# Optimization experiments

Hardware: AMD Instinct MI355X
Metric: run time of the kernel (lower is better)

## Reference

```python
import jax, jax.numpy as jnp
import numpy as np

N_NODES = 100000
N_EDGES = 1600000
IN_DIM = 48
HID = 128
BN_EPS = 1e-5


def _batchnorm(h, gamma, beta):
    # BatchNorm1d in training mode: batch mean, biased variance
    mu = jnp.mean(h, axis=0)
    var = jnp.mean(jnp.square(h - mu), axis=0)
    return (h - mu) * jax.lax.rsqrt(var + BN_EPS) * gamma + beta


def setup_inputs() -> dict:
    key = jax.random.key(0)
    ks = jax.random.split(key, 8)
    x = jax.random.normal(ks[0], (N_NODES, IN_DIM), dtype=jnp.float32)
    edge_index = jax.random.randint(ks[1], (2, N_EDGES), 0, N_NODES, dtype=jnp.int64)
    s1 = 1.0 / np.sqrt(IN_DIM)
    s2 = 1.0 / np.sqrt(HID)
    return {
        "x": x,
        "edge_index": edge_index,
        "W1": jax.random.uniform(ks[2], (HID, IN_DIM), jnp.float32, -s1, s1),
        "b1": jnp.zeros((HID,), jnp.float32),
        "g1": jnp.ones((HID,), jnp.float32),
        "be1": jnp.zeros((HID,), jnp.float32),
        "Wl": jax.random.uniform(ks[3], (HID, HID), jnp.float32, -s2, s2),
        "bl": jnp.zeros((HID,), jnp.float32),
        "Wr": jax.random.uniform(ks[4], (HID, HID), jnp.float32, -s2, s2),
        "g2": jnp.ones((HID,), jnp.float32),
        "be2": jnp.zeros((HID,), jnp.float32),
    }


def reference(x, edge_index, W1, b1, g1, be1, Wl, bl, Wr, g2, be2):
    # input projection: Linear -> BatchNorm -> ReLU
    h = x @ W1.T + b1                               # [N, HID]
    feat = jax.nn.relu(_batchnorm(h, g1, be1))      # [N, HID]

    # SAGEConv (mean aggregation): messages flow src -> dst
    src, dst = edge_index[0], edge_index[1]
    summed = jax.ops.segment_sum(feat[src], dst, num_segments=N_NODES)  # [N, HID]
    cnt = jax.ops.segment_sum(jnp.ones((N_EDGES,), jnp.float32), dst, num_segments=N_NODES)
    agg = summed / jnp.maximum(cnt, 1.0)[:, None]
    sage = agg @ Wl.T + bl + feat @ Wr.T            # lin_l(mean) + lin_r(self)

    out_feat = _batchnorm(sage, g2, be2)
    return (feat, out_feat)
```

## Files before the change

kernel.cpp:

```cpp
#include <hip/hip_runtime.h>
#include <hip/hip_bf16.h>

#define NN 100000
#define NE 1600000
#define INDIM 48
#define HID 128
#define K2 256
#define KP 64
#define BN_EPS 1e-5f

#define NBUK 782
#define BCAP 2816
#define CHUNK 8192
#define NBB 196
#define NPRJ 320

#define MT2 ((NN + 127) / 128)

typedef short s8v __attribute__((ext_vector_type(8)));
typedef float f4v __attribute__((ext_vector_type(4)));
typedef float f2v __attribute__((ext_vector_type(2)));

__device__ __forceinline__ unsigned short f2bf(float f) {
    __hip_bfloat16 b = __float2bfloat16(f);
    unsigned short u;
    __builtin_memcpy(&u, &b, 2);
    return u;
}
__device__ __forceinline__ float bflo(unsigned u) { return __uint_as_float(u << 16); }
__device__ __forceinline__ float bfhi(unsigned u) { return __uint_as_float(u & 0xffff0000u); }
__device__ __forceinline__ unsigned packbf(float lo, float hi) {
    return (unsigned)f2bf(lo) | ((unsigned)f2bf(hi) << 16);
}

__global__ __launch_bounds__(512) void k_prep_proj(const int* __restrict__ ei,
                                                   int* __restrict__ bcur,
                                                   unsigned int* __restrict__ bbuf,
                                                   const float* __restrict__ x,
                                                   const float* __restrict__ W1,
                                                   const float* __restrict__ b1,
                                                   unsigned short* __restrict__ Abuf,
                                                   float* __restrict__ colSum,
                                                   float* __restrict__ colSq) {
  union __align__(16) SMem {
    struct {
      int cnt[1024];
      int sc[2][1024];
      int ofs[1024];
      int lcur[1024];
      int gbase[1024];
      unsigned int stag[CHUNK];
      unsigned short sbkt[CHUNK];
    } p;
    struct {
      unsigned short Bsh[HID][KP + 8];
      float redS[8][HID];
      float redQ[8][HID];
    } g;
  };
  __shared__ SMem sm;
  int tid = threadIdx.x;

  if (blockIdx.x < NBB) {
    int base = blockIdx.x * CHUNK;
    int lim = min(CHUNK, NE - base);
    sm.p.cnt[tid] = 0;
    sm.p.cnt[tid + 512] = 0;
    __syncthreads();
#pragma unroll
    for (int i = 0; i < CHUNK / 512; ++i) {
      int e = i * 512 + tid;
      if (e < lim) {
        int d = ei[NE + base + e];
        d = min(max(d, 0), NN - 1);
        atomicAdd(&sm.p.cnt[d >> 7], 1);
      }
    }
    __syncthreads();
    sm.p.sc[0][tid] = sm.p.cnt[tid];
    sm.p.sc[0][tid + 512] = sm.p.cnt[tid + 512];
    __syncthreads();
    int pp = 0;
    for (int d = 1; d < 1024; d <<= 1) {
      int a0 = sm.p.sc[pp][tid];
      int a1 = sm.p.sc[pp][tid + 512];
      if (tid >= d) a0 += sm.p.sc[pp][tid - d];
      a1 += sm.p.sc[pp][tid + 512 - d];
      sm.p.sc[pp ^ 1][tid] = a0;
      sm.p.sc[pp ^ 1][tid + 512] = a1;
      __syncthreads();
      pp ^= 1;
    }
    sm.p.ofs[tid] = sm.p.sc[pp][tid] - sm.p.cnt[tid];
    sm.p.ofs[tid + 512] = sm.p.sc[pp][tid + 512] - sm.p.cnt[tid + 512];
    sm.p.lcur[tid] = sm.p.ofs[tid];
    sm.p.lcur[tid + 512] = sm.p.ofs[tid + 512];
    if (tid < NBUK) sm.p.gbase[tid] = atomicAdd(&bcur[tid], sm.p.cnt[tid]);
    if (tid + 512 < NBUK) sm.p.gbase[tid + 512] = atomicAdd(&bcur[tid + 512], sm.p.cnt[tid + 512]);
    __syncthreads();
#pragma unroll
    for (int i = 0; i < CHUNK / 512; ++i) {
      int e = i * 512 + tid;
      if (e < lim) {
        int s = ei[base + e];
        int d = ei[NE + base + e];
        s = min(max(s, 0), NN - 1);
        d = min(max(d, 0), NN - 1);
        int b = d >> 7;
        int pos = atomicAdd(&sm.p.lcur[b], 1);
        sm.p.stag[pos] = (unsigned)s | ((unsigned)(d & 127) << 17);
        sm.p.sbkt[pos] = (unsigned short)b;
      }
    }
    __syncthreads();
    for (int s = tid; s < lim; s += 512) {
      int b = sm.p.sbkt[s];
      int off = sm.p.gbase[b] + (s - sm.p.ofs[b]);
      if (off < BCAP) bbuf[(size_t)b * BCAP + off] = sm.p.stag[s];
    }
    return;
  }

  int bid2 = blockIdx.x - NBB;
  for (int i = tid; i < HID * KP; i += 512) {
    int j = i >> 6, k = i & (KP - 1);
    sm.g.Bsh[j][k] = (k < INDIM) ? f2bf(W1[j * INDIM + k]) : (unsigned short)0;
  }
  __syncthreads();
  int w = tid >> 6, l = tid & 63;
  int m16 = l & 15, q = l >> 4;
  float bcol[8];
#pragma unroll
  for (int nt = 0; nt < 8; ++nt) bcol[nt] = b1[nt * 16 + m16];
  float ssum[8], ssq[8];
#pragma unroll
  for (int nt = 0; nt < 8; ++nt) { ssum[nt] = 0.f; ssq[nt] = 0.f; }
  f4v zero4 = {0.f, 0.f, 0.f, 0.f};
  s8v zero8 = {0, 0, 0, 0, 0, 0, 0, 0};
  for (int tile = bid2; tile < MT2; tile += NPRJ) {
    int row = tile * 128 + w * 16 + m16;
    bool rv = row < NN;
    const float* xr = x + (size_t)row * INDIM;
    f4v acc[8];
#pragma unroll
    for (int nt = 0; nt < 8; ++nt) acc[nt] = zero4;
#pragma unroll
    for (int kt = 0; kt < 2; ++kt) {
      int c0 = kt * 32 + q * 8;
      s8v a = zero8;
      if (rv && c0 < INDIM) {
        float4 v0 = *(const float4*)(xr + c0);
        float4 v1 = *(const float4*)(xr + c0 + 4);
        a[0] = (short)f2bf(v0.x); a[1] = (short)f2bf(v0.y);
        a[2] = (short)f2bf(v0.z); a[3] = (short)f2bf(v0.w);
        a[4] = (short)f2bf(v1.x); a[5] = (short)f2bf(v1.y);
        a[6] = (short)f2bf(v1.z); a[7] = (short)f2bf(v1.w);
      }
#pragma unroll
      for (int nt = 0; nt < 8; ++nt) {
        s8v b = *(const s8v*)(&sm.g.Bsh[nt * 16 + m16][kt * 32 + q * 8]);
        acc[nt] = __builtin_amdgcn_mfma_f32_16x16x32_bf16(a, b, acc[nt], 0, 0, 0);
      }
    }
    int rbase = tile * 128 + w * 16 + q * 4;
#pragma unroll
    for (int nt = 0; nt < 8; ++nt) {
      int col = nt * 16 + m16;
#pragma unroll
      for (int r4 = 0; r4 < 4; ++r4) {
        int rr = rbase + r4;
        if (rr < NN) {
          float v = acc[nt][r4] + bcol[nt];
          Abuf[(size_t)rr * K2 + HID + col] = f2bf(v);
          ssum[nt] += v;
          ssq[nt] = fmaf(v, v, ssq[nt]);
        }
      }
    }
  }
#pragma unroll
  for (int nt = 0; nt < 8; ++nt) {
    float s = ssum[nt], qq = ssq[nt];
    s += __shfl_xor(s, 16);
    s += __shfl_xor(s, 32);
    qq += __shfl_xor(qq, 16);
    qq += __shfl_xor(qq, 32);
    if (q == 0) {
      sm.g.redS[w][nt * 16 + m16] = s;
      sm.g.redQ[w][nt * 16 + m16] = qq;
    }
  }
  __syncthreads();
  if (tid < HID) {
    float s = 0.f, qq = 0.f;
#pragma unroll
    for (int ww = 0; ww < 8; ++ww) { s += sm.g.redS[ww][tid]; qq += sm.g.redQ[ww][tid]; }
    atomicAdd(&colSum[tid], s);
    atomicAdd(&colSq[tid], qq);
  }
}

__global__ __launch_bounds__(256) void k_apply(float* __restrict__ feat,
                                               const float* __restrict__ colSum,
                                               const float* __restrict__ colSq,
                                               const float* __restrict__ g1,
                                               const float* __restrict__ be1,
                                               unsigned short* __restrict__ A,
                                               unsigned char* __restrict__ feat8) {
  __shared__ __align__(16) float sa[HID], sb[HID];
  int tid = threadIdx.x;
  if (tid < HID) {
    float mu = colSum[tid] * (1.0f / NN);
    float var = fmaxf(colSq[tid] * (1.0f / NN) - mu * mu, 0.f);
    float a = g1[tid] * rsqrtf(var + BN_EPS);
    sa[tid] = a;
    sb[tid] = be1[tid] - mu * a;
  }
  __syncthreads();
  int i = blockIdx.x * 256 + tid;
  if (i >= NN * 16) return;
  int r = i >> 4, c8 = (i & 15) << 3;
  unsigned short* ap = A + (size_t)r * K2 + HID + c8;
  uint4 hv = *(const uint4*)ap;
  float4 a0 = *(const float4*)(sa + c8);
  float4 a1 = *(const float4*)(sa + c8 + 4);
  float4 b0 = *(const float4*)(sb + c8);
  float4 b1 = *(const float4*)(sb + c8 + 4);
  float f0 = fmaxf(fmaf(bflo(hv.x), a0.x, b0.x), 0.f);
  float f1 = fmaxf(fmaf(bfhi(hv.x), a0.y, b0.y), 0.f);
  float f2 = fmaxf(fmaf(bflo(hv.y), a0.z, b0.z), 0.f);
  float f3 = fmaxf(fmaf(bfhi(hv.y), a0.w, b0.w), 0.f);
  float f4 = fmaxf(fmaf(bflo(hv.z), a1.x, b1.x), 0.f);
  float f5 = fmaxf(fmaf(bfhi(hv.z), a1.y, b1.y), 0.f);
  float f6 = fmaxf(fmaf(bflo(hv.w), a1.z, b1.z), 0.f);
  float f7 = fmaxf(fmaf(bfhi(hv.w), a1.w, b1.w), 0.f);
  float4 o0 = {f0, f1, f2, f3}, o1 = {f4, f5, f6, f7};
  *(float4*)(feat + (size_t)r * HID + c8) = o0;
  *(float4*)(feat + (size_t)r * HID + c8 + 4) = o1;
  uint4 ob;
  ob.x = packbf(f0, f1);
  ob.y = packbf(f2, f3);
  ob.z = packbf(f4, f5);
  ob.w = packbf(f6, f7);
  *(uint4*)ap = ob;
  unsigned p0 = __builtin_amdgcn_cvt_pk_fp8_f32(f0, f1, 0u, false);
  p0 = __builtin_amdgcn_cvt_pk_fp8_f32(f2, f3, p0, true);
  unsigned p1 = __builtin_amdgcn_cvt_pk_fp8_f32(f4, f5, 0u, false);
  p1 = __builtin_amdgcn_cvt_pk_fp8_f32(f6, f7, p1, true);
  uint2 o8 = {p0, p1};
  *(uint2*)(feat8 + (size_t)r * HID + c8) = o8;
}

__global__ __launch_bounds__(512) void k_bucket_agg(const unsigned int* __restrict__ bbuf,
                                                    const int* __restrict__ bcnt,
                                                    const unsigned char* __restrict__ feat8,
                                                    unsigned short* __restrict__ Abuf) {
  __shared__ unsigned int lcsr[BCAP];
  __shared__ int cnt[128], ofs[128], cur[128];
  __shared__ int sc[2][128];
  int tid = threadIdx.x;
  int b = blockIdx.x;
  int m = min(bcnt[b], BCAP);
  int n0 = b << 7;
  int nb = min(128, NN - n0);
  if (tid < 128) cnt[tid] = 0;
  __syncthreads();
  const unsigned int* bp = bbuf + (size_t)b * BCAP;
  for (int s = tid; s < m; s += 512) {
    unsigned p = bp[s];
    atomicAdd(&cnt[(p >> 17) & 127], 1);
  }
  __syncthreads();
  if (tid < 128) sc[0][tid] = cnt[tid];
  __syncthreads();
  int pp = 0;
  for (int d = 1; d < 128; d <<= 1) {
    if (tid < 128) {
      int v = sc[pp][tid];
      if (tid >= d) v += sc[pp][tid - d];
      sc[pp ^ 1][tid] = v;
    }
    __syncthreads();
    pp ^= 1;
  }
  if (tid < 128) {
    int o = sc[pp][tid] - cnt[tid];
    ofs[tid] = o;
    cur[tid] = o;
  }
  __syncthreads();
  for (int s = tid; s < m; s += 512) {
    unsigned p = bp[s];
    int ld = (p >> 17) & 127;
    int pos = atomicAdd(&cur[ld], 1);
    lcsr[pos] = p & 0x1FFFF;
  }
  __syncthreads();
  int lane = tid & 31;
  int g = tid >> 5;
  int half = (lane >> 3) & 3;
  int l8 = lane & 7;
  for (int ln = g; ln < nb; ln += 16) {
    int deg = cnt[ln], beg = ofs[ln];
    float ac[16];
#pragma unroll
    for (int i = 0; i < 16; ++i) ac[i] = 0.f;
#pragma unroll 2
    for (int j = 0; j < deg; j += 4) {
      int idx = j + half;
      uint4 v = {0u, 0u, 0u, 0u};
      if (idx < deg) {
        int s = lcsr[beg + idx];
        v = *(const uint4*)(feat8 + (size_t)s * HID + l8 * 16);
      }
      f2v d;
      d = __builtin_amdgcn_cvt_pk_f32_fp8(v.x, false); ac[0] += d.x;  ac[1] += d.y;
      d = __builtin_amdgcn_cvt_pk_f32_fp8(v.x, true);  ac[2] += d.x;  ac[3] += d.y;
      d = __builtin_amdgcn_cvt_pk_f32_fp8(v.y, false); ac[4] += d.x;  ac[5] += d.y;
      d = __builtin_amdgcn_cvt_pk_f32_fp8(v.y, true);  ac[6] += d.x;  ac[7] += d.y;
      d = __builtin_amdgcn_cvt_pk_f32_fp8(v.z, false); ac[8] += d.x;  ac[9] += d.y;
      d = __builtin_amdgcn_cvt_pk_f32_fp8(v.z, true);  ac[10] += d.x; ac[11] += d.y;
      d = __builtin_amdgcn_cvt_pk_f32_fp8(v.w, false); ac[12] += d.x; ac[13] += d.y;
      d = __builtin_amdgcn_cvt_pk_f32_fp8(v.w, true);  ac[14] += d.x; ac[15] += d.y;
    }
#pragma unroll
    for (int i = 0; i < 16; ++i) {
      ac[i] += __shfl_xor(ac[i], 8);
      ac[i] += __shfl_xor(ac[i], 16);
    }
    if (half == 0) {
      float inv = 1.f / fmaxf((float)deg, 1.f);
      uint4 o0, o1;
      o0.x = packbf(ac[0] * inv, ac[1] * inv);
      o0.y = packbf(ac[2] * inv, ac[3] * inv);
      o0.z = packbf(ac[4] * inv, ac[5] * inv);
      o0.w = packbf(ac[6] * inv, ac[7] * inv);
      o1.x = packbf(ac[8] * inv, ac[9] * inv);
      o1.y = packbf(ac[10] * inv, ac[11] * inv);
      o1.z = packbf(ac[12] * inv, ac[13] * inv);
      o1.w = packbf(ac[14] * inv, ac[15] * inv);
      unsigned short* op = Abuf + (size_t)(n0 + ln) * K2 + l8 * 16;
      *(uint4*)op = o0;
      *(uint4*)(op + 8) = o1;
    }
  }
}

__global__ __launch_bounds__(512) void k_gemm(
    const unsigned short* __restrict__ A,
    const float* __restrict__ Wl, const float* __restrict__ Wr,
    const float* __restrict__ bl, unsigned short* __restrict__ sageb,
    float* __restrict__ colSum, float* __restrict__ colSq) {
  __shared__ __align__(16) unsigned short Bsh[HID][264];
  __shared__ float redS[8][HID], redQ[8][HID];
  int tid = threadIdx.x;
  for (int i4 = tid; i4 < HID * K2 / 4; i4 += 512) {
    int i = i4 << 2;
    int j = i >> 8, k = i & (K2 - 1);
    const float* src = (k < HID) ? (Wl + j * HID + k) : (Wr + j * HID + (k - HID));
    float4 v = *(const float4*)src;
    uint2 u;
    u.x = packbf(v.x, v.y);
    u.y = packbf(v.z, v.w);
    *(uint2*)&Bsh[j][k] = u;
  }
  __syncthreads();
  int w = tid >> 6, l = tid & 63;
  int m16 = l & 15, q = l >> 4;
  int tile = blockIdx.x;
  int row = tile * 128 + w * 16 + m16;
  bool rv = row < NN;
  f4v zero4 = {0.f, 0.f, 0.f, 0.f};
  s8v zero8 = {0, 0, 0, 0, 0, 0, 0, 0};
  f4v acc[8];
#pragma unroll
  for (int nt = 0; nt < 8; ++nt) acc[nt] = zero4;
#pragma unroll
  for (int kt = 0; kt < 8; ++kt) {
    s8v a = zero8;
    if (rv) a = *(const s8v*)(A + (size_t)row * K2 + kt * 32 + q * 8);
#pragma unroll
    for (int nt = 0; nt < 8; ++nt) {
      s8v bfr = *(const s8v*)(&Bsh[nt * 16 + m16][kt * 32 + q * 8]);
      acc[nt] = __builtin_amdgcn_mfma_f32_16x16x32_bf16(a, bfr, acc[nt], 0, 0, 0);
    }
  }
  int rbase = tile * 128 + w * 16 + q * 4;
  float ssum[8], ssq[8];
#pragma unroll
  for (int nt = 0; nt < 8; ++nt) { ssum[nt] = 0.f; ssq[nt] = 0.f; }
#pragma unroll
  for (int nt = 0; nt < 8; ++nt) {
    int col = nt * 16 + m16;
    float bv = bl[col];
#pragma unroll
    for (int r4 = 0; r4 < 4; ++r4) {
      int rr = rbase + r4;
      if (rr < NN) {
        float v = acc[nt][r4] + bv;
        sageb[(size_t)rr * HID + col] = f2bf(v);
        ssum[nt] += v;
        ssq[nt] = fmaf(v, v, ssq[nt]);
      }
    }
  }
#pragma unroll
  for (int nt = 0; nt < 8; ++nt) {
    float s = ssum[nt], qq = ssq[nt];
    s += __shfl_xor(s, 16);
    s += __shfl_xor(s, 32);
    qq += __shfl_xor(qq, 16);
    qq += __shfl_xor(qq, 32);
    if (q == 0) {
      redS[w][nt * 16 + m16] = s;
      redQ[w][nt * 16 + m16] = qq;
    }
  }
  __syncthreads();
  if (tid < HID) {
    float s = 0.f, qq = 0.f;
#pragma unroll
    for (int ww = 0; ww < 8; ++ww) { s += redS[ww][tid]; qq += redQ[ww][tid]; }
    atomicAdd(&colSum[tid], s);
    atomicAdd(&colSq[tid], qq);
  }
}

__global__ __launch_bounds__(256) void k_bn_apply(const unsigned short* __restrict__ sageb,
                                                  float* __restrict__ out,
                                                  const float* __restrict__ colSum,
                                                  const float* __restrict__ colSq,
                                                  const float* __restrict__ g2,
                                                  const float* __restrict__ be2) {
  __shared__ __align__(16) float sa[HID], sb[HID];
  int tid = threadIdx.x;
  if (tid < HID) {
    float mu = colSum[tid] * (1.0f / NN);
    float var = fmaxf(colSq[tid] * (1.0f / NN) - mu * mu, 0.f);
    float a = g2[tid] * rsqrtf(var + BN_EPS);
    sa[tid] = a;
    sb[tid] = be2[tid] - mu * a;
  }
  __syncthreads();
  int i = blockIdx.x * 256 + tid;
  if (i >= NN * 16) return;
  int r = i >> 4, c8 = (i & 15) << 3;
  uint4 sv = *(const uint4*)(sageb + (size_t)r * HID + c8);
  float4 a0 = *(const float4*)(sa + c8);
  float4 a1 = *(const float4*)(sa + c8 + 4);
  float4 b0 = *(const float4*)(sb + c8);
  float4 b1 = *(const float4*)(sb + c8 + 4);
  float4 o0, o1;
  o0.x = fmaf(bflo(sv.x), a0.x, b0.x);
  o0.y = fmaf(bfhi(sv.x), a0.y, b0.y);
  o0.z = fmaf(bflo(sv.y), a0.z, b0.z);
  o0.w = fmaf(bfhi(sv.y), a0.w, b0.w);
  o1.x = fmaf(bflo(sv.z), a1.x, b1.x);
  o1.y = fmaf(bfhi(sv.z), a1.y, b1.y);
  o1.z = fmaf(bflo(sv.w), a1.z, b1.z);
  o1.w = fmaf(bfhi(sv.w), a1.w, b1.w);
  *(float4*)(out + (size_t)r * HID + c8) = o0;
  *(float4*)(out + (size_t)r * HID + c8 + 4) = o1;
}

extern "C" void kernel_launch(void* const* d_in, const int* in_sizes, int n_in,
                              void* d_out, int out_size, void* d_ws, size_t ws_size,
                              hipStream_t stream) {
  const float* x   = (const float*)d_in[0];
  const int*   ei  = (const int*)d_in[1];
  const float* W1  = (const float*)d_in[2];
  const float* b1  = (const float*)d_in[3];
  const float* g1  = (const float*)d_in[4];
  const float* be1 = (const float*)d_in[5];
  const float* Wl  = (const float*)d_in[6];
  const float* bl  = (const float*)d_in[7];
  const float* Wr  = (const float*)d_in[8];
  const float* g2  = (const float*)d_in[9];
  const float* be2 = (const float*)d_in[10];

  float* feat_out = (float*)d_out;
  float* out2     = (float*)d_out + (size_t)NN * HID;

  size_t off = 0;
  auto alloc = [&](size_t bytes) -> void* {
    void* p = (char*)d_ws + off;
    off += (bytes + 255) & ~(size_t)255;
    return p;
  };
  float*          stats = (float*)alloc(4 * HID * 4);
  int*            bcur  = (int*)alloc((size_t)NBUK * 4);
  unsigned short* Abuf  = (unsigned short*)alloc((size_t)NN * K2 * 2);
  unsigned char*  feat8 = (unsigned char*)alloc((size_t)NN * HID);
  unsigned short* sageb = (unsigned short*)alloc((size_t)NN * HID * 2);
  unsigned int*   bbuf  = (unsigned int*)alloc((size_t)NBUK * BCAP * 4);
  float* colSum1 = stats;
  float* colSq1  = stats + HID;
  float* colSum2 = stats + 2 * HID;
  float* colSq2  = stats + 3 * HID;

  hipMemsetAsync(stats, 0, 4 * HID * 4 + (size_t)NBUK * 4, stream);
  k_prep_proj<<<NBB + NPRJ, 512, 0, stream>>>(ei, bcur, bbuf, x, W1, b1, Abuf, colSum1, colSq1);
  k_apply<<<(NN * 16 + 255) / 256, 256, 0, stream>>>(feat_out, colSum1, colSq1, g1, be1, Abuf, feat8);
  k_bucket_agg<<<NBUK, 512, 0, stream>>>(bbuf, bcur, feat8, Abuf);
  k_gemm<<<MT2, 512, 0, stream>>>(Abuf, Wl, Wr, bl, sageb, colSum2, colSq2);
  k_bn_apply<<<(NN * 16 + 255) / 256, 256, 0, stream>>>(sageb, out2, colSum2, colSq2, g2, be2);
}
```

Baseline: 287.3 us.

## Fuse neighbor aggregation with SAGE GEMM, keep aggregated tile in LDS

Merges the bucket aggregation kernel and the SAGE GEMM into one kernel. Each block writes its 128-node mean-aggregated tile into shared memory and feeds it straight into MFMA, so the aggregate is never written to or read back from global memory. The self-feature buffer shrinks from 256 to 128 columns, and the concatenated Wl/Wr weights are converted to bf16 once by extra blocks in the prep kernel. In exchange, the GEMM now reads B fragments directly from global/L2 instead of LDS, and the fused kernel uses more shared memory and registers, which may reduce occupancy.

```diff
diff --git a/kernel.cpp b/kernel.cpp
--- a/kernel.cpp
+++ b/kernel.cpp
@@ -14,6 +14,7 @@
 #define CHUNK 8192
 #define NBB 196
 #define NPRJ 320
+#define NWC 4
 
 #define MT2 ((NN + 127) / 128)
 
@@ -41,7 +42,10 @@
                                                    const float* __restrict__ b1,
                                                    unsigned short* __restrict__ Abuf,
                                                    float* __restrict__ colSum,
-                                                   float* __restrict__ colSq) {
+                                                   float* __restrict__ colSq,
+                                                   const float* __restrict__ Wl,
+                                                   const float* __restrict__ Wr,
+                                                   unsigned short* __restrict__ Wcat) {
   union __align__(16) SMem {
     struct {
       int cnt[1024];
@@ -61,6 +65,21 @@
   __shared__ SMem sm;
   int tid = threadIdx.x;
 
+  if (blockIdx.x >= NBB + NPRJ) {
+    int t0 = (blockIdx.x - NBB - NPRJ) * 512 + tid;
+    for (int i4 = t0; i4 < HID * K2 / 4; i4 += NWC * 512) {
+      int i = i4 << 2;
+      int j = i >> 8, k = i & (K2 - 1);
+      const float* src = (k < HID) ? (Wl + j * HID + k) : (Wr + j * HID + (k - HID));
+      float4 v = *(const float4*)src;
+      uint2 u;
+      u.x = packbf(v.x, v.y);
+      u.y = packbf(v.z, v.w);
+      *(uint2*)(Wcat + i) = u;
+    }
+    return;
+  }
+
   if (blockIdx.x < NBB) {
     int base = blockIdx.x * CHUNK;
     int lim = min(CHUNK, NE - base);
@@ -171,7 +190,7 @@
         int rr = rbase + r4;
         if (rr < NN) {
           float v = acc[nt][r4] + bcol[nt];
-          Abuf[(size_t)rr * K2 + HID + col] = f2bf(v);
+          Abuf[(size_t)rr * HID + col] = f2bf(v);
           ssum[nt] += v;
           ssq[nt] = fmaf(v, v, ssq[nt]);
         }
@@ -220,7 +239,7 @@
   int i = blockIdx.x * 256 + tid;
   if (i >= NN * 16) return;
   int r = i >> 4, c8 = (i & 15) << 3;
-  unsigned short* ap = A + (size_t)r * K2 + HID + c8;
+  unsigned short* ap = A + (size_t)r * HID + c8;
   uint4 hv = *(const uint4*)ap;
   float4 a0 = *(const float4*)(sa + c8);
   float4 a1 = *(const float4*)(sa + c8 + 4);
@@ -251,19 +270,26 @@
   *(uint2*)(feat8 + (size_t)r * HID + c8) = o8;
 }
 
-__global__ __launch_bounds__(512) void k_bucket_agg(const unsigned int* __restrict__ bbuf,
-                                                    const int* __restrict__ bcnt,
-                                                    const unsigned char* __restrict__ feat8,
-                                                    unsigned short* __restrict__ Abuf) {
+__global__ __launch_bounds__(512, 4) void k_agg_gemm(const unsigned int* __restrict__ bbuf,
+                                                     const int* __restrict__ bcnt,
+                                                     const unsigned char* __restrict__ feat8,
+                                                     const unsigned short* __restrict__ Abuf,
+                                                     const unsigned short* __restrict__ Wcat,
+                                                     const float* __restrict__ bl,
+                                                     unsigned short* __restrict__ sageb,
+                                                     float* __restrict__ colSum,
+                                                     float* __restrict__ colSq) {
   __shared__ unsigned int lcsr[BCAP];
   __shared__ int cnt[128], ofs[128], cur[128];
   __shared__ int sc[2][128];
+  __shared__ __align__(16) unsigned short aggL[128][136];
+  __shared__ float sS[HID], sQ[HID];
   int tid = threadIdx.x;
   int b = blockIdx.x;
   int m = min(bcnt[b], BCAP);
   int n0 = b << 7;
   int nb = min(128, NN - n0);
-  if (tid < 128) cnt[tid] = 0;
+  if (tid < 128) { cnt[tid] = 0; sS[tid] = 0.f; sQ[tid] = 0.f; }
   __syncthreads();
   const unsigned int* bp = bbuf + (size_t)b * BCAP;
   for (int s = tid; s < m; s += 512) {
@@ -296,79 +322,60 @@
     lcsr[pos] = p & 0x1FFFF;
   }
   __syncthreads();
-  int lane = tid & 31;
-  int g = tid >> 5;
-  int half = (lane >> 3) & 3;
-  int l8 = lane & 7;
-  for (int ln = g; ln < nb; ln += 16) {
-    int deg = cnt[ln], beg = ofs[ln];
-    float ac[16];
-#pragma unroll
-    for (int i = 0; i < 16; ++i) ac[i] = 0.f;
+  {
+    int lane = tid & 31;
+    int g = tid >> 5;
+    int half = (lane >> 3) & 3;
+    int l8 = lane & 7;
+    for (int ln = g; ln < nb; ln += 16) {
+      int deg = cnt[ln], beg = ofs[ln];
+      float ac[16];
+#pragma unroll
+      for (int i = 0; i < 16; ++i) ac[i] = 0.f;
 #pragma unroll 2
-    for (int j = 0; j < deg; j += 4) {
-      int idx = j + half;
-      uint4 v = {0u, 0u, 0u, 0u};
-      if (idx < deg) {
-        int s = lcsr[beg + idx];
-        v = *(const uint4*)(feat8 + (size_t)s * HID + l8 * 16);
-      }
-      f2v d;
-      d = __builtin_amdgcn_cvt_pk_f32_fp8(v.x, false); ac[0] += d.x;  ac[1] += d.y;
-      d = __builtin_amdgcn_cvt_pk_f32_fp8(v.x, true);  ac[2] += d.x;  ac[3] += d.y;
-      d = __builtin_amdgcn_cvt_pk_f32_fp8(v.y, false); ac[4] += d.x;  ac[5] += d.y;
-      d = __builtin_amdgcn_cvt_pk_f32_fp8(v.y, true);  ac[6] += d.x;  ac[7] += d.y;
-      d = __builtin_amdgcn_cvt_pk_f32_fp8(v.z, false); ac[8] += d.x;  ac[9] += d.y;
-      d = __builtin_amdgcn_cvt_pk_f32_fp8(v.z, true);  ac[10] += d.x; ac[11] += d.y;
-      d = __builtin_amdgcn_cvt_pk_f32_fp8(v.w, false); ac[12] += d.x; ac[13] += d.y;
-      d = __builtin_amdgcn_cvt_pk_f32_fp8(v.w, true);  ac[14] += d.x; ac[15] += d.y;
-    }
-#pragma unroll
-    for (int i = 0; i < 16; ++i) {
-      ac[i] += __shfl_xor(ac[i], 8);
-      ac[i] += __shfl_xor(ac[i], 16);
-    }
-    if (half == 0) {
-      float inv = 1.f / fmaxf((float)deg, 1.f);
-      uint4 o0, o1;
-      o0.x = packbf(ac[0] * inv, ac[1] * inv);
-      o0.y = packbf(ac[2] * inv, ac[3] * inv);
-      o0.z = packbf(ac[4] * inv, ac[5] * inv);
-      o0.w = packbf(ac[6] * inv, ac[7] * inv);
-      o1.x = packbf(ac[8] * inv, ac[9] * inv);
-      o1.y = packbf(ac[10] * inv, ac[11] * inv);
-      o1.z = packbf(ac[12] * inv, ac[13] * inv);
-      o1.w = packbf(ac[14] * inv, ac[15] * inv);
-      unsigned short* op = Abuf + (size_t)(n0 + ln) * K2 + l8 * 16;
-      *(uint4*)op = o0;
-      *(uint4*)(op + 8) = o1;
-    }
-  }
-}
-
-__global__ __launch_bounds__(512) void k_gemm(
-    const unsigned short* __restrict__ A,
-    const float* __restrict__ Wl, const float* __restrict__ Wr,
-    const float* __restrict__ bl, unsigned short* __restrict__ sageb,
-    float* __restrict__ colSum, float* __restrict__ colSq) {
-  __shared__ __align__(16) unsigned short Bsh[HID][264];
-  __shared__ float redS[8][HID], redQ[8][HID];
-  int tid = threadIdx.x;
-  for (int i4 = tid; i4 < HID * K2 / 4; i4 += 512) {
-    int i = i4 << 2;
-    int j = i >> 8, k = i & (K2 - 1);
-    const float* src = (k < HID) ? (Wl + j * HID + k) : (Wr + j * HID + (k - HID));
-    float4 v = *(const float4*)src;
-    uint2 u;
-    u.x = packbf(v.x, v.y);
-    u.y = packbf(v.z, v.w);
-    *(uint2*)&Bsh[j][k] = u;
+      for (int j = 0; j < deg; j += 4) {
+        int idx = j + half;
+        uint4 v = {0u, 0u, 0u, 0u};
+        if (idx < deg) {
+          int s = lcsr[beg + idx];
+          v = *(const uint4*)(feat8 + (size_t)s * HID + l8 * 16);
+        }
+        f2v d;
+        d = __builtin_amdgcn_cvt_pk_f32_fp8(v.x, false); ac[0] += d.x;  ac[1] += d.y;
+        d = __builtin_amdgcn_cvt_pk_f32_fp8(v.x, true);  ac[2] += d.x;  ac[3] += d.y;
+        d = __builtin_amdgcn_cvt_pk_f32_fp8(v.y, false); ac[4] += d.x;  ac[5] += d.y;
+        d = __builtin_amdgcn_cvt_pk_f32_fp8(v.y, true);  ac[6] += d.x;  ac[7] += d.y;
+        d = __builtin_amdgcn_cvt_pk_f32_fp8(v.z, false); ac[8] += d.x;  ac[9] += d.y;
+        d = __builtin_amdgcn_cvt_pk_f32_fp8(v.z, true);  ac[10] += d.x; ac[11] += d.y;
+        d = __builtin_amdgcn_cvt_pk_f32_fp8(v.w, false); ac[12] += d.x; ac[13] += d.y;
+        d = __builtin_amdgcn_cvt_pk_f32_fp8(v.w, true);  ac[14] += d.x; ac[15] += d.y;
+      }
+#pragma unroll
+      for (int i = 0; i < 16; ++i) {
+        ac[i] += __shfl_xor(ac[i], 8);
+        ac[i] += __shfl_xor(ac[i], 16);
+      }
+      if (half == 0) {
+        float inv = 1.f / fmaxf((float)deg, 1.f);
+        uint4 o0, o1;
+        o0.x = packbf(ac[0] * inv, ac[1] * inv);
+        o0.y = packbf(ac[2] * inv, ac[3] * inv);
+        o0.z = packbf(ac[4] * inv, ac[5] * inv);
+        o0.w = packbf(ac[6] * inv, ac[7] * inv);
+        o1.x = packbf(ac[8] * inv, ac[9] * inv);
+        o1.y = packbf(ac[10] * inv, ac[11] * inv);
+        o1.z = packbf(ac[12] * inv, ac[13] * inv);
+        o1.w = packbf(ac[14] * inv, ac[15] * inv);
+        unsigned short* op = &aggL[ln][l8 * 16];
+        *(uint4*)op = o0;
+        *(uint4*)(op + 8) = o1;
+      }
+    }
   }
   __syncthreads();
   int w = tid >> 6, l = tid & 63;
   int m16 = l & 15, q = l >> 4;
-  int tile = blockIdx.x;
-  int row = tile * 128 + w * 16 + m16;
+  int row = n0 + w * 16 + m16;
   bool rv = row < NN;
   f4v zero4 = {0.f, 0.f, 0.f, 0.f};
   s8v zero8 = {0, 0, 0, 0, 0, 0, 0, 0};
@@ -377,15 +384,20 @@
   for (int nt = 0; nt < 8; ++nt) acc[nt] = zero4;
 #pragma unroll
   for (int kt = 0; kt < 8; ++kt) {
-    s8v a = zero8;
-    if (rv) a = *(const s8v*)(A + (size_t)row * K2 + kt * 32 + q * 8);
+    s8v a;
+    if (kt < 4) {
+      a = *(const s8v*)(&aggL[w * 16 + m16][kt * 32 + q * 8]);
+      if (!rv) a = zero8;
+    } else {
+      a = rv ? *(const s8v*)(Abuf + (size_t)row * HID + (kt - 4) * 32 + q * 8) : zero8;
+    }
 #pragma unroll
     for (int nt = 0; nt < 8; ++nt) {
-      s8v bfr = *(const s8v*)(&Bsh[nt * 16 + m16][kt * 32 + q * 8]);
+      s8v bfr = *(const s8v*)(Wcat + (size_t)(nt * 16 + m16) * K2 + kt * 32 + q * 8);
       acc[nt] = __builtin_amdgcn_mfma_f32_16x16x32_bf16(a, bfr, acc[nt], 0, 0, 0);
     }
   }
-  int rbase = tile * 128 + w * 16 + q * 4;
+  int rbase = n0 + w * 16 + q * 4;
   float ssum[8], ssq[8];
 #pragma unroll
   for (int nt = 0; nt < 8; ++nt) { ssum[nt] = 0.f; ssq[nt] = 0.f; }
@@ -412,17 +424,14 @@
     qq += __shfl_xor(qq, 16);
     qq += __shfl_xor(qq, 32);
     if (q == 0) {
-      redS[w][nt * 16 + m16] = s;
-      redQ[w][nt * 16 + m16] = qq;
+      atomicAdd(&sS[nt * 16 + m16], s);
+      atomicAdd(&sQ[nt * 16 + m16], qq);
     }
   }
   __syncthreads();
   if (tid < HID) {
-    float s = 0.f, qq = 0.f;
-#pragma unroll
-    for (int ww = 0; ww < 8; ++ww) { s += redS[ww][tid]; qq += redQ[ww][tid]; }
-    atomicAdd(&colSum[tid], s);
-    atomicAdd(&colSq[tid], qq);
+    atomicAdd(&colSum[tid], sS[tid]);
+    atomicAdd(&colSq[tid], sQ[tid]);
   }
 }
 
@@ -489,19 +498,20 @@
   };
   float*          stats = (float*)alloc(4 * HID * 4);
   int*            bcur  = (int*)alloc((size_t)NBUK * 4);
-  unsigned short* Abuf  = (unsigned short*)alloc((size_t)NN * K2 * 2);
+  unsigned short* Abuf  = (unsigned short*)alloc((size_t)NN * HID * 2);
   unsigned char*  feat8 = (unsigned char*)alloc((size_t)NN * HID);
   unsigned short* sageb = (unsigned short*)alloc((size_t)NN * HID * 2);
   unsigned int*   bbuf  = (unsigned int*)alloc((size_t)NBUK * BCAP * 4);
+  unsigned short* Wcat  = (unsigned short*)alloc((size_t)HID * K2 * 2);
   float* colSum1 = stats;
   float* colSq1  = stats + HID;
   float* colSum2 = stats + 2 * HID;
   float* colSq2  = stats + 3 * HID;
 
   hipMemsetAsync(stats, 0, 4 * HID * 4 + (size_t)NBUK * 4, stream);
-  k_prep_proj<<<NBB + NPRJ, 512, 0, stream>>>(ei, bcur, bbuf, x, W1, b1, Abuf, colSum1, colSq1);
+  k_prep_proj<<<NBB + NPRJ + NWC, 512, 0, stream>>>(ei, bcur, bbuf, x, W1, b1, Abuf,
+                                                    colSum1, colSq1, Wl, Wr, Wcat);
   k_apply<<<(NN * 16 + 255) / 256, 256, 0, stream>>>(feat_out, colSum1, colSq1, g1, be1, Abuf, feat8);
-  k_bucket_agg<<<NBUK, 512, 0, stream>>>(bbuf, bcur, feat8, Abuf);
-  k_gemm<<<MT2, 512, 0, stream>>>(Abuf, Wl, Wr, bl, sageb, colSum2, colSq2);
+  k_agg_gemm<<<NBUK, 512, 0, stream>>>(bbuf, bcur, feat8, Abuf, Wcat, bl, sageb, colSum2, colSq2);
   k_bn_apply<<<(NN * 16 + 255) / 256, 256, 0, stream>>>(sageb, out2, colSum2, colSq2, g2, be2);
 }
```

Result: slower. 336.0 us (+16.9%).
